# Optimization experiments

Measured on AMD Instinct MI355X. Metric: run time of the kernel, lower is better.

Reference implementation:

```python
import jax, jax.numpy as jnp
import numpy as np
from jax import lax

ACT_SCALE = (0.5, 0.5, 0.5)  # act_scale[0..2], also used as bias_scale
STRIDE = 2
QLEVELS = 127.0  # int8 fake-quant levels (2**7 - 1)


@jax.custom_vjp
def ste_round(x):
    return jnp.round(x)

def _ste_fwd(x):
    return jnp.round(x), None

def _ste_bwd(_, g):
    return (g,)

ste_round.defvjp(_ste_fwd, _ste_bwd)


def fq_act(x, scale):
    # quantize_activations_gemm_A: normalize by scale, clip to [-1,1], 8-bit grid
    return ste_round(jnp.clip(x / scale, -1.0, 1.0) * QLEVELS) / QLEVELS


def qw(w):
    # quantize_weight_gemm_S: per-tensor max-abs scale + 8-bit fake quant
    s = jnp.max(jnp.abs(w))
    wq = ste_round(jnp.clip(w / s, -1.0, 1.0) * QLEVELS) / QLEVELS
    return wq, s


def qb(b):
    # quantize_bias_gemm: round to 1/127 grid
    return ste_round(b * QLEVELS) / QLEVELS


def relu6s(x, scale):
    # ReLU6S: scaled ReLU6
    return jnp.clip(x / scale, 0.0, 6.0)


def conv(x, w, stride=1, pad=0):
    return lax.conv_general_dilated(
        x, w, (stride, stride), [(pad, pad), (pad, pad)],
        dimension_numbers=("NCHW", "OIHW", "NCHW"))


def bottleneck_fwd(x, w1, b1, w2, b2, w3, b3, ws, bs):
    s0, s1, s2a = ACT_SCALE
    x = fq_act(x, s0)
    residual = x
    # conv1: 1x1
    w1q, c1s = qw(w1)
    b1q = qb(b1) / (c1s * s0)
    out = (conv(x, w1q) + b1q[None, :, None, None]) * c1s
    out = relu6s(out, s0) * s0
    out = fq_act(out, s1)
    # conv2: 3x3 stride
    w2q, c2s = qw(w2)
    b2q = qb(b2) / (c2s * s1)
    out = (conv(out, w2q, stride=STRIDE, pad=1) + b2q[None, :, None, None]) * c2s
    out = relu6s(out, s1) * s1
    out = fq_act(out, s2a)
    # conv3: 1x1 (source's padding=1 on a 1x1 conv is a shape bug; dropped)
    w3q, c3s = qw(w3)
    b3q = qb(b3) / (c2s * s2a)  # NOTE: source divides by conv2_scale (preserved)
    out = (conv(out, w3q) + b3q[None, :, None, None]) * c3s
    out = out * s2a
    # downsample shortcut: 1x1 stride
    wsq, css = qw(ws)
    bsq = qb(bs) / (css * s0)
    residual = (conv(residual, wsq, stride=STRIDE) + bsq[None, :, None, None]) * css
    residual = residual * s0
    return jnp.clip(out + residual, 0.0, 6.0)  # final ReLU6


def setup_inputs() -> dict:
    key = jax.random.key(0)
    ks = jax.random.split(key, 9)
    B, Cin, P, H, W = 64, 512, 256, 28, 28
    Cout = 4 * P
    def w_init(k, shape):
        fan_in = shape[1] * shape[2] * shape[3]
        return jax.random.normal(k, shape, jnp.float32) * np.float32(np.sqrt(2.0 / fan_in))
    return {
        "x": jax.random.normal(ks[0], (B, Cin, H, W), jnp.float32),
        "w1": w_init(ks[1], (P, Cin, 1, 1)),
        "b1": jax.random.normal(ks[2], (P,), jnp.float32) * 0.01,
        "w2": w_init(ks[3], (P, P, 3, 3)),
        "b2": jax.random.normal(ks[4], (P,), jnp.float32) * 0.01,
        "w3": w_init(ks[5], (Cout, P, 1, 1)),
        "b3": jax.random.normal(ks[6], (Cout,), jnp.float32) * 0.01,
        "ws": w_init(ks[7], (Cout, Cin, 1, 1)),
        "bs": jax.random.normal(ks[8], (Cout,), jnp.float32) * 0.01,
    }


def reference(x, w1, b1, w2, b2, w3, b3, ws, bs):
    return bottleneck_fwd(x, w1, b1, w2, b2, w3, b3, ws, bs)
```

## Files before the change

### kernel.cpp

```cpp
#include <hip/hip_runtime.h>
#include <stdint.h>

typedef int   int4v __attribute__((ext_vector_type(4)));
typedef float f32x4 __attribute__((ext_vector_type(4)));

#define WS_SCALES 0ull
#define WS_ZERO   256ull
#define WS_BI1    1024ull
#define WS_BI2    2048ull
#define WS_BI3    4096ull
#define WS_BIS    8192ull
#define WS_W1Q    16384ull
#define WS_W2Q    (WS_W1Q + 131072ull)
#define WS_W3Q    (WS_W2Q + 589824ull)
#define WS_WSQ    (WS_W3Q + 262144ull)
#define WS_A0     2097152ull
#define WS_A1     (WS_A0 + 25690112ull)
#define WS_A2     (WS_A1 + 12845056ull)

__device__ __forceinline__ void gll16(const void* g, void* l) {
    __builtin_amdgcn_global_load_lds((const __attribute__((address_space(1))) void*)g,
                                     (__attribute__((address_space(3))) void*)l, 16, 0, 0);
}

#define VMCNT_BAR(n) asm volatile("s_waitcnt vmcnt(" #n ")\n\ts_barrier" ::: "memory")

__global__ void k_init(float* wshead) {
    int i = blockIdx.x * 256 + threadIdx.x;
    wshead[i] = 0.0f;
}

__global__ void k_maxabs(const float* __restrict__ w1, const float* __restrict__ w2,
                         const float* __restrict__ w3, const float* __restrict__ wsd,
                         float* __restrict__ scales) {
    const float* srcs[4] = {w1, w2, w3, wsd};
    const int n4s[4] = {32768, 147456, 65536, 131072};
    int t = blockIdx.y;
    const f32x4* s = (const f32x4*)srcs[t];
    int n4 = n4s[t];
    float m = 0.0f;
    for (int i = blockIdx.x * 256 + threadIdx.x; i < n4; i += gridDim.x * 256) {
        f32x4 v = s[i];
        m = fmaxf(m, fmaxf(fmaxf(fabsf(v[0]), fabsf(v[1])), fmaxf(fabsf(v[2]), fabsf(v[3]))));
    }
    __shared__ float red[256];
    red[threadIdx.x] = m;
    __syncthreads();
    for (int st = 128; st > 0; st >>= 1) {
        if (threadIdx.x < st) red[threadIdx.x] = fmaxf(red[threadIdx.x], red[threadIdx.x + st]);
        __syncthreads();
    }
    if (threadIdx.x == 0) atomicMax((int*)&scales[t], __float_as_int(red[0]));
}

__global__ void k_quant_w(const float* __restrict__ w1, const float* __restrict__ w2,
                          const float* __restrict__ w3, const float* __restrict__ wsd,
                          const float* __restrict__ b1, const float* __restrict__ b2,
                          const float* __restrict__ b3, const float* __restrict__ bs,
                          char* __restrict__ wsb) {
    const float* sc = (const float*)(wsb + WS_SCALES);
    int mode = blockIdx.y;
    int i0 = blockIdx.x * 256 + threadIdx.x;
    int stride = gridDim.x * 256;
    if (mode == 0) {
        float s = sc[0]; signed char* o = (signed char*)(wsb + WS_W1Q);
        for (int i = i0; i < 131072; i += stride)
            o[i] = (signed char)(int)rintf(fminf(fmaxf(w1[i] / s, -1.f), 1.f) * 127.f);
    } else if (mode == 1) {
        float s = sc[1]; signed char* o = (signed char*)(wsb + WS_W2Q);
        for (int i = i0; i < 589824; i += stride) {
            int oo = i / 2304, r2 = i - oo * 2304;
            int c = r2 / 9, kk = r2 - c * 9;
            o[(size_t)oo * 2304 + kk * 256 + c] =
                (signed char)(int)rintf(fminf(fmaxf(w2[i] / s, -1.f), 1.f) * 127.f);
        }
    } else if (mode == 2) {
        float s = sc[2]; signed char* o = (signed char*)(wsb + WS_W3Q);
        for (int i = i0; i < 262144; i += stride)
            o[i] = (signed char)(int)rintf(fminf(fmaxf(w3[i] / s, -1.f), 1.f) * 127.f);
    } else if (mode == 3) {
        float s = sc[3]; signed char* o = (signed char*)(wsb + WS_WSQ);
        for (int i = i0; i < 524288; i += stride)
            o[i] = (signed char)(int)rintf(fminf(fmaxf(wsd[i] / s, -1.f), 1.f) * 127.f);
    } else if (mode == 4) {
        float* o = (float*)(wsb + WS_BI1);
        for (int i = i0; i < 256; i += stride) o[i] = rintf(b1[i] * 127.f);
    } else if (mode == 5) {
        float* o = (float*)(wsb + WS_BI2);
        for (int i = i0; i < 256; i += stride) o[i] = rintf(b2[i] * 127.f);
    } else if (mode == 6) {
        float* o = (float*)(wsb + WS_BI3);
        for (int i = i0; i < 1024; i += stride) o[i] = rintf(b3[i] * 127.f);
    } else {
        float* o = (float*)(wsb + WS_BIS);
        for (int i = i0; i < 1024; i += stride) o[i] = rintf(bs[i] * 127.f);
    }
}

__global__ __launch_bounds__(256) void k_quant_x(const float* __restrict__ x,
                                                 signed char* __restrict__ a0) {
    __shared__ signed char tile[32][132];
    int b = blockIdx.z;
    int p0 = blockIdx.x * 128, c0 = blockIdx.y * 32;
    int tc = threadIdx.x >> 3;
    int pq = (threadIdx.x & 7) * 16;
    const float* xr = x + ((size_t)b * 512 + c0 + tc) * 784 + p0 + pq;
#pragma unroll
    for (int u = 0; u < 4; u++) {
        int p = p0 + pq + u * 4;
        f32x4 v = {0.f, 0.f, 0.f, 0.f};
        if (p < 784) v = *(const f32x4*)(xr + u * 4);
        signed char q[4];
#pragma unroll
        for (int e = 0; e < 4; e++) {
            float f = fminf(fmaxf(v[e] * 2.f, -1.f), 1.f);
            q[e] = (signed char)(int)rintf(f * 127.f);
        }
        *(int*)&tile[tc][pq + u * 4] = *(int*)q;
    }
    __syncthreads();
#pragma unroll
    for (int u = 0; u < 4; u++) {
        int idx = threadIdx.x + u * 256;
        int pp = idx >> 3, cs = (idx & 7) * 4;
        if (p0 + pp < 784) {
            unsigned pk = 0;
#pragma unroll
            for (int i = 0; i < 4; i++)
                pk |= (unsigned)(unsigned char)tile[cs + i][pp] << (8 * i);
            *(unsigned*)(a0 + ((size_t)b * 784 + p0 + pp) * 512 + c0 + cs) = pk;
        }
    }
}

template <int MODE, int BM, int BN, int WGM, int WGN>
__global__ __launch_bounds__(256) void k_conv(char* __restrict__ wsb, float* __restrict__ dout) {
    constexpr int FM = BM / WGM / 16;
    constexpr int FN = BN / WGN / 16;
    constexpr int SB = BN / 16;
    constexpr int NI_B = SB / 4;
    constexpr int KTOT = (MODE == 0) ? 512 : (MODE == 1) ? 2304 : 768;
    constexpr int NSTEP = KTOT / 64;
    constexpr int BMP = BM + 16;
    constexpr int LDS_STAGE = BN * 64;
    constexpr int LDS_EPI = (MODE == 2) ? 64 * (BN + 4) * 4 : BN * BMP;
    constexpr int LDSZ = (3 * LDS_STAGE > LDS_EPI) ? 3 * LDS_STAGE : LDS_EPI;
    static_assert(FM + NI_B == 6 || FM + NI_B == 4, "steady bar count");
    static_assert(FM == 4 || FM == 2, "tail bar count");
    static_assert(NSTEP % 2 == 0, "even steps");

    __shared__ alignas(16) char lds[LDSZ];

    const int tid = threadIdx.x;
    const int wid = tid >> 6;
    const int lane = tid & 63;
    const int n0 = blockIdx.x * BN;
    const int m0 = blockIdx.y * BM;
    const int bb = blockIdx.z;

    const float* sc = (const float*)(wsb + WS_SCALES);
    const int srow = lane >> 2;
    const int lrow = lane & 15;
    const int quad = lane >> 4;
    const int wm = (wid % WGM) * (BM / WGM);
    const int wn = (wid / WGM) * (BN / WGN);
    const int xco = ((lane & 3) ^ ((lane >> 3) & 3)) << 4;
    const char* zp = wsb + WS_ZERO + xco;

    const char* aB[FM];
    const char* aB2[FM];
#pragma unroll
    for (int i = 0; i < FM; i++) {
        int m = m0 + wm + i * 16 + lrow;
        if constexpr (MODE == 0) {
            aB[i] = wsb + WS_W1Q + (size_t)m * 512 + quad * 16;
        } else if constexpr (MODE == 1) {
            aB[i] = wsb + WS_W2Q + (size_t)m * 2304 + quad * 16;
        } else {
            aB[i]  = wsb + WS_W3Q + (size_t)m * 256 + quad * 16;
            aB2[i] = wsb + WS_WSQ + (size_t)m * 512 + quad * 16;
        }
    }

    int4v acc3[FM][FN] = {};
    int4v accS[FM][FN] = {};

    auto srcB = [&](int s, int k0) -> const char* {
        int n = n0 + s * 16 + srow;
        const char* g = zp;
        if constexpr (MODE == 0) {
            g = wsb + WS_A0 + (size_t)n * 512 + k0 + xco;
        } else if constexpr (MODE == 1) {
            unsigned b = (unsigned)n / 196u;
            unsigned hw = (unsigned)n - b * 196u;
            int oh = hw / 14, ow = hw - oh * 14;
            int tap = k0 >> 8;
            int kh = tap / 3, kw = tap - kh * 3;
            int c0 = k0 & 255;
            int ih = 2 * oh - 1 + kh, iw = 2 * ow - 1 + kw;
            if (ih >= 0 && ih < 28 && iw >= 0 && iw < 28)
                g = wsb + WS_A1 + ((size_t)b * 784 + ih * 28 + iw) * 256 + c0 + xco;
        } else {
            if (n < 196) {
                if (k0 < 256) {
                    g = wsb + WS_A2 + ((size_t)bb * 196 + n) * 256 + k0 + xco;
                } else {
                    int oh = n / 14, ow = n - oh * 14;
                    int ps = oh * 56 + ow * 2;
                    g = wsb + WS_A0 + ((size_t)bb * 784 + ps) * 512 + (k0 - 256) + xco;
                }
            }
        }
        return g;
    };

    auto stageB = [&](int t, char* buf) {
        const int k0 = t * 64;
#pragma unroll
        for (int ii = 0; ii < NI_B; ii++) {
            const int s = wid + ii * 4;
            gll16(srcB(s, k0), buf + s * 1024);
        }
    };

    auto loadA = [&](int t, int4v (&a)[FM]) {
        if constexpr (MODE == 2) {
            if (t < 4) {
                const int off = t * 64;
#pragma unroll
                for (int i = 0; i < FM; i++) a[i] = *(const int4v*)(aB[i] + off);
            } else {
                const int off = (t - 4) * 64;
#pragma unroll
                for (int i = 0; i < FM; i++) a[i] = *(const int4v*)(aB2[i] + off);
            }
        } else {
            const int off = t * 64;
#pragma unroll
            for (int i = 0; i < FM; i++) a[i] = *(const int4v*)(aB[i] + off);
        }
    };

    auto dsB = [&](const char* cur, int4v (&b)[FN]) {
#pragma unroll
        for (int j = 0; j < FN; j++) {
            int n = wn + j * 16 + lrow;
            b[j] = *(const int4v*)(cur + n * 64 + ((quad ^ ((n >> 1) & 3)) << 4));
        }
    };

    auto MF = [&](int4v (&ac)[FM][FN], int4v (&a)[FM], int4v (&b)[FN]) {
#pragma unroll
        for (int i = 0; i < FM; i++)
#pragma unroll
            for (int j = 0; j < FN; j++)
                ac[i][j] = __builtin_amdgcn_mfma_i32_16x16x64_i8(a[i], b[j], ac[i][j], 0, 0, 0);
    };

    int4v aC[FM], aN[FM], bfr[FN];
    stageB(0, lds);
    stageB(1, lds + LDS_STAGE);
    loadA(0, aC);
    VMCNT_BAR(0);

    for (int t = 0; t < NSTEP; t += 2) {
        loadA(t + 1, aN);
        __builtin_amdgcn_sched_barrier(0);
        if (t + 2 < NSTEP) stageB(t + 2, lds + ((t + 2) % 3) * LDS_STAGE);
        dsB(lds + (t % 3) * LDS_STAGE, bfr);
        if (MODE != 2 || t < 4) MF(acc3, aC, bfr); else MF(accS, aC, bfr);
        if (t + 1 == NSTEP - 1) {
            if constexpr (FM == 4) VMCNT_BAR(4); else VMCNT_BAR(2);
        } else {
            if constexpr (FM + NI_B == 6) VMCNT_BAR(6); else VMCNT_BAR(4);
        }

        if (t + 2 < NSTEP) loadA(t + 2, aC);
        __builtin_amdgcn_sched_barrier(0);
        if (t + 3 < NSTEP) stageB(t + 3, lds + ((t + 3) % 3) * LDS_STAGE);
        dsB(lds + ((t + 1) % 3) * LDS_STAGE, bfr);
        if (MODE != 2 || t + 1 < 4) MF(acc3, aN, bfr); else MF(accS, aN, bfr);
        if (t + 2 < NSTEP) {
            if constexpr (FM + NI_B == 6) VMCNT_BAR(6); else VMCNT_BAR(4);
        }
    }

    if constexpr (MODE == 0 || MODE == 1) {
        const float alpha = sc[MODE] / 16129.0f;
        const float* bi = (const float*)(wsb + (MODE == 0 ? WS_BI1 : WS_BI2));
        signed char* outp = (signed char*)(wsb + (MODE == 0 ? WS_A1 : WS_A2));
        __syncthreads();
#pragma unroll
        for (int i = 0; i < FM; i++) {
            int mloc = wm + i * 16 + quad * 4;
            int mb = m0 + mloc;
            float bt[4];
#pragma unroll
            for (int r = 0; r < 4; r++) bt[r] = bi[mb + r] * (2.0f / 127.0f);
#pragma unroll
            for (int j = 0; j < FN; j++) {
                int nloc = wn + j * 16 + lrow;
                unsigned pk = 0;
#pragma unroll
                for (int r = 0; r < 4; r++) {
                    float v = alpha * (float)acc3[i][j][r] + bt[r];
                    int q = (int)rintf(127.0f * fminf(fmaxf(2.0f * v, 0.0f), 1.0f));
                    pk |= (unsigned)(q & 0xFF) << (8 * r);
                }
                *(unsigned*)(lds + nloc * BMP + mloc) = pk;
            }
        }
        __syncthreads();
        for (int u = tid; u < BN * (BM / 16); u += 256) {
            int row = u / (BM / 16);
            int seg = u % (BM / 16);
            uint4 v = *(const uint4*)(lds + row * BMP + seg * 16);
            *(uint4*)(outp + (size_t)(n0 + row) * 256 + m0 + seg * 16) = v;
        }
    } else {
        const float c2 = sc[1], c3 = sc[2], cS = sc[3];
        const float* bi3 = (const float*)(wsb + WS_BI3);
        const float* bis = (const float*)(wsb + WS_BIS);
        float* ldsF = (float*)lds;
        constexpr int LDN = BN + 4;
        constexpr int SEGS = BN / 16;
        for (int half = 0; half < 2; half++) {
            __syncthreads();
            if (wm == half * 64) {
#pragma unroll
                for (int i = 0; i < FM; i++) {
                    int mloc = i * 16 + quad * 4;
                    int mg = m0 + half * 64 + mloc;
                    float bt[4];
#pragma unroll
                    for (int r = 0; r < 4; r++)
                        bt[r] = bi3[mg + r] * (c3 / (127.0f * c2)) + bis[mg + r] * (1.0f / 127.0f);
#pragma unroll
                    for (int j = 0; j < FN; j++) {
                        int nloc = wn + j * 16 + lrow;
#pragma unroll
                        for (int r = 0; r < 4; r++) {
                            float v = (c3 * (float)acc3[i][j][r] + cS * (float)accS[i][j][r])
                                          * (0.5f / 16129.0f) + bt[r];
                            v = v < 0.0f ? 0.0f : (v > 6.0f ? 6.0f : v);
                            ldsF[(mloc + r) * LDN + nloc] = v;
                        }
                    }
                }
            }
            __syncthreads();
            {
                int rw0 = tid / SEGS, seg = tid % SEGS;
                int nbase = n0 + seg * 16;
                for (int row = rw0; row < 64; row += 256 / SEGS) {
                    const float* src = ldsF + row * LDN + seg * 16;
                    float* dst = dout + ((size_t)bb * 1024 + m0 + half * 64 + row) * 196 + nbase;
                    if (nbase + 16 <= 196) {
                        *(f32x4*)(dst + 0)  = *(const f32x4*)(src + 0);
                        *(f32x4*)(dst + 4)  = *(const f32x4*)(src + 4);
                        *(f32x4*)(dst + 8)  = *(const f32x4*)(src + 8);
                        *(f32x4*)(dst + 12) = *(const f32x4*)(src + 12);
                    } else {
                        for (int q = 0; q < 16 && nbase + q < 196; q++) dst[q] = src[q];
                    }
                }
            }
        }
    }
}

extern "C" void kernel_launch(void* const* d_in, const int* in_sizes, int n_in,
                              void* d_out, int out_size, void* d_ws, size_t ws_size,
                              hipStream_t stream) {
    const float* x   = (const float*)d_in[0];
    const float* w1  = (const float*)d_in[1];
    const float* b1  = (const float*)d_in[2];
    const float* w2  = (const float*)d_in[3];
    const float* b2  = (const float*)d_in[4];
    const float* w3  = (const float*)d_in[5];
    const float* b3  = (const float*)d_in[6];
    const float* wsd = (const float*)d_in[7];
    const float* bs  = (const float*)d_in[8];
    float* out = (float*)d_out;
    char* wsb = (char*)d_ws;

    k_init<<<16, 256, 0, stream>>>((float*)wsb);
    k_maxabs<<<dim3(128, 4), 256, 0, stream>>>(w1, w2, w3, wsd, (float*)(wsb + WS_SCALES));
    k_quant_w<<<dim3(96, 8), 256, 0, stream>>>(w1, w2, w3, wsd, b1, b2, b3, bs, wsb);
    k_quant_x<<<dim3(7, 16, 64), 256, 0, stream>>>(x, (signed char*)(wsb + WS_A0));
    k_conv<0, 128, 128, 2, 2><<<dim3(392, 2, 1), 256, 0, stream>>>(wsb, out);
    k_conv<1, 64, 128, 2, 2><<<dim3(98, 4, 1), 256, 0, stream>>>(wsb, out);
    k_conv<2, 128, 128, 2, 2><<<dim3(2, 8, 64), 256, 0, stream>>>(wsb, out);
}
```

Measured before the change: 334.9 us.

## Stage whole K in LDS for 1x1 convs; LDS-stage both operands in 3x3 conv

The 1x1 conv kernels (conv1 and conv3+shortcut) now issue every B-tile load for the full K range up front into LDS, wait once, then run all MFMAs with A read straight from global. This drops the hand-tuned triple-buffer pipeline and its per-step waits. The 3x3 conv moves to its own kernel that stages both weights and im2col activations through a triple-buffered LDS ring with a single wait per step. The trade-off is much larger LDS use in the 1x1 kernels (up to 96KB for MODE 2), which lowers occupancy and loses the overlap of loads with compute.

```diff
diff --git a/kernel.cpp b/kernel.cpp
--- a/kernel.cpp
+++ b/kernel.cpp
@@ -134,20 +134,17 @@
 }
 
 template <int MODE, int BM, int BN, int WGM, int WGN>
-__global__ __launch_bounds__(256) void k_conv(char* __restrict__ wsb, float* __restrict__ dout) {
+__global__ __launch_bounds__(256) void k_conv_os(char* __restrict__ wsb, float* __restrict__ dout) {
     constexpr int FM = BM / WGM / 16;
     constexpr int FN = BN / WGN / 16;
-    constexpr int SB = BN / 16;
-    constexpr int NI_B = SB / 4;
-    constexpr int KTOT = (MODE == 0) ? 512 : (MODE == 1) ? 2304 : 768;
+    constexpr int NI_B = BN / 64;
+    constexpr int KTOT = (MODE == 0) ? 512 : 768;
     constexpr int NSTEP = KTOT / 64;
     constexpr int BMP = BM + 16;
     constexpr int LDS_STAGE = BN * 64;
+    constexpr int LDS_ALL = NSTEP * LDS_STAGE;
     constexpr int LDS_EPI = (MODE == 2) ? 64 * (BN + 4) * 4 : BN * BMP;
-    constexpr int LDSZ = (3 * LDS_STAGE > LDS_EPI) ? 3 * LDS_STAGE : LDS_EPI;
-    static_assert(FM + NI_B == 6 || FM + NI_B == 4, "steady bar count");
-    static_assert(FM == 4 || FM == 2, "tail bar count");
-    static_assert(NSTEP % 2 == 0, "even steps");
+    constexpr int LDSZ = (LDS_ALL > LDS_EPI) ? LDS_ALL : LDS_EPI;
 
     __shared__ alignas(16) char lds[LDSZ];
 
@@ -174,56 +171,44 @@
         int m = m0 + wm + i * 16 + lrow;
         if constexpr (MODE == 0) {
             aB[i] = wsb + WS_W1Q + (size_t)m * 512 + quad * 16;
-        } else if constexpr (MODE == 1) {
-            aB[i] = wsb + WS_W2Q + (size_t)m * 2304 + quad * 16;
         } else {
             aB[i]  = wsb + WS_W3Q + (size_t)m * 256 + quad * 16;
             aB2[i] = wsb + WS_WSQ + (size_t)m * 512 + quad * 16;
         }
     }
 
+#pragma unroll
+    for (int t = 0; t < NSTEP; t++) {
+        const int k0 = t * 64;
+#pragma unroll
+        for (int ii = 0; ii < NI_B; ii++) {
+            const int s = wid + ii * 4;
+            int n = n0 + s * 16 + srow;
+            const char* g = zp;
+            if constexpr (MODE == 0) {
+                g = wsb + WS_A0 + (size_t)n * 512 + k0 + xco;
+            } else {
+                if (n < 196) {
+                    if (k0 < 256) {
+                        g = wsb + WS_A2 + ((size_t)bb * 196 + n) * 256 + k0 + xco;
+                    } else {
+                        int oh = n / 14, ow = n - oh * 14;
+                        int ps = oh * 56 + ow * 2;
+                        g = wsb + WS_A0 + ((size_t)bb * 784 + ps) * 512 + (k0 - 256) + xco;
+                    }
+                }
+            }
+            gll16(g, lds + t * LDS_STAGE + s * 1024);
+        }
+    }
+    VMCNT_BAR(0);
+
     int4v acc3[FM][FN] = {};
     int4v accS[FM][FN] = {};
 
-    auto srcB = [&](int s, int k0) -> const char* {
-        int n = n0 + s * 16 + srow;
-        const char* g = zp;
-        if constexpr (MODE == 0) {
-            g = wsb + WS_A0 + (size_t)n * 512 + k0 + xco;
-        } else if constexpr (MODE == 1) {
-            unsigned b = (unsigned)n / 196u;
-            unsigned hw = (unsigned)n - b * 196u;
-            int oh = hw / 14, ow = hw - oh * 14;
-            int tap = k0 >> 8;
-            int kh = tap / 3, kw = tap - kh * 3;
-            int c0 = k0 & 255;
-            int ih = 2 * oh - 1 + kh, iw = 2 * ow - 1 + kw;
-            if (ih >= 0 && ih < 28 && iw >= 0 && iw < 28)
-                g = wsb + WS_A1 + ((size_t)b * 784 + ih * 28 + iw) * 256 + c0 + xco;
-        } else {
-            if (n < 196) {
-                if (k0 < 256) {
-                    g = wsb + WS_A2 + ((size_t)bb * 196 + n) * 256 + k0 + xco;
-                } else {
-                    int oh = n / 14, ow = n - oh * 14;
-                    int ps = oh * 56 + ow * 2;
-                    g = wsb + WS_A0 + ((size_t)bb * 784 + ps) * 512 + (k0 - 256) + xco;
-                }
-            }
-        }
-        return g;
-    };
-
-    auto stageB = [&](int t, char* buf) {
-        const int k0 = t * 64;
-#pragma unroll
-        for (int ii = 0; ii < NI_B; ii++) {
-            const int s = wid + ii * 4;
-            gll16(srcB(s, k0), buf + s * 1024);
-        }
-    };
-
-    auto loadA = [&](int t, int4v (&a)[FM]) {
+#pragma unroll
+    for (int t = 0; t < NSTEP; t++) {
+        int4v a[FM], b[FN];
         if constexpr (MODE == 2) {
             if (t < 4) {
                 const int off = t * 64;
@@ -239,56 +224,31 @@
 #pragma unroll
             for (int i = 0; i < FM; i++) a[i] = *(const int4v*)(aB[i] + off);
         }
-    };
-
-    auto dsB = [&](const char* cur, int4v (&b)[FN]) {
+        const char* cur = lds + t * LDS_STAGE;
 #pragma unroll
         for (int j = 0; j < FN; j++) {
             int n = wn + j * 16 + lrow;
             b[j] = *(const int4v*)(cur + n * 64 + ((quad ^ ((n >> 1) & 3)) << 4));
         }
-    };
-
-    auto MF = [&](int4v (&ac)[FM][FN], int4v (&a)[FM], int4v (&b)[FN]) {
-#pragma unroll
-        for (int i = 0; i < FM; i++)
-#pragma unroll
-            for (int j = 0; j < FN; j++)
-                ac[i][j] = __builtin_amdgcn_mfma_i32_16x16x64_i8(a[i], b[j], ac[i][j], 0, 0, 0);
-    };
-
-    int4v aC[FM], aN[FM], bfr[FN];
-    stageB(0, lds);
-    stageB(1, lds + LDS_STAGE);
-    loadA(0, aC);
-    VMCNT_BAR(0);
-
-    for (int t = 0; t < NSTEP; t += 2) {
-        loadA(t + 1, aN);
-        __builtin_amdgcn_sched_barrier(0);
-        if (t + 2 < NSTEP) stageB(t + 2, lds + ((t + 2) % 3) * LDS_STAGE);
-        dsB(lds + (t % 3) * LDS_STAGE, bfr);
-        if (MODE != 2 || t < 4) MF(acc3, aC, bfr); else MF(accS, aC, bfr);
-        if (t + 1 == NSTEP - 1) {
-            if constexpr (FM == 4) VMCNT_BAR(4); else VMCNT_BAR(2);
+        if (MODE != 2 || t < 4) {
+#pragma unroll
+            for (int i = 0; i < FM; i++)
+#pragma unroll
+                for (int j = 0; j < FN; j++)
+                    acc3[i][j] = __builtin_amdgcn_mfma_i32_16x16x64_i8(a[i], b[j], acc3[i][j], 0, 0, 0);
         } else {
-            if constexpr (FM + NI_B == 6) VMCNT_BAR(6); else VMCNT_BAR(4);
-        }
-
-        if (t + 2 < NSTEP) loadA(t + 2, aC);
-        __builtin_amdgcn_sched_barrier(0);
-        if (t + 3 < NSTEP) stageB(t + 3, lds + ((t + 3) % 3) * LDS_STAGE);
-        dsB(lds + ((t + 1) % 3) * LDS_STAGE, bfr);
-        if (MODE != 2 || t + 1 < 4) MF(acc3, aN, bfr); else MF(accS, aN, bfr);
-        if (t + 2 < NSTEP) {
-            if constexpr (FM + NI_B == 6) VMCNT_BAR(6); else VMCNT_BAR(4);
-        }
-    }
-
-    if constexpr (MODE == 0 || MODE == 1) {
-        const float alpha = sc[MODE] / 16129.0f;
-        const float* bi = (const float*)(wsb + (MODE == 0 ? WS_BI1 : WS_BI2));
-        signed char* outp = (signed char*)(wsb + (MODE == 0 ? WS_A1 : WS_A2));
+#pragma unroll
+            for (int i = 0; i < FM; i++)
+#pragma unroll
+                for (int j = 0; j < FN; j++)
+                    accS[i][j] = __builtin_amdgcn_mfma_i32_16x16x64_i8(a[i], b[j], accS[i][j], 0, 0, 0);
+        }
+    }
+
+    if constexpr (MODE == 0) {
+        const float alpha = sc[0] / 16129.0f;
+        const float* bi = (const float*)(wsb + WS_BI1);
+        signed char* outp = (signed char*)(wsb + WS_A1);
         __syncthreads();
 #pragma unroll
         for (int i = 0; i < FM; i++) {
@@ -369,6 +329,129 @@
     }
 }
 
+__global__ __launch_bounds__(256) void k_conv2(char* __restrict__ wsb) {
+    constexpr int BM = 64, BN = 128, WGM = 2, WGN = 2;
+    constexpr int FM = BM / WGM / 16;
+    constexpr int FN = BN / WGN / 16;
+    constexpr int ISS_A = BM / 16;
+    constexpr int NI = (BM + BN) / 64;
+    constexpr int NSTEP = 2304 / 64;
+    constexpr int BMP = BM + 16;
+    constexpr int LDS_STAGE = (BM + BN) * 64;
+    constexpr int LDS_EPI = BN * BMP;
+    constexpr int LDSZ = 3 * LDS_STAGE;
+
+    __shared__ alignas(16) char lds[LDSZ];
+
+    const int tid = threadIdx.x;
+    const int wid = tid >> 6;
+    const int lane = tid & 63;
+    const int n0 = blockIdx.x * BN;
+    const int m0 = blockIdx.y * BM;
+
+    const float* sc = (const float*)(wsb + WS_SCALES);
+    const int srow = lane >> 2;
+    const int lrow = lane & 15;
+    const int quad = lane >> 4;
+    const int wm = (wid % WGM) * (BM / WGM);
+    const int wn = (wid / WGM) * (BN / WGN);
+    const int xco = ((lane & 3) ^ ((lane >> 3) & 3)) << 4;
+    const char* zp = wsb + WS_ZERO + xco;
+
+    int4v acc[FM][FN] = {};
+
+    auto src_ptr = [&](int s, int k0) -> const char* {
+        const char* g;
+        if (s < ISS_A) {
+            int m = m0 + s * 16 + srow;
+            g = wsb + WS_W2Q + (size_t)m * 2304 + k0 + xco;
+        } else {
+            int n = n0 + (s - ISS_A) * 16 + srow;
+            g = zp;
+            unsigned b = (unsigned)n / 196u;
+            unsigned hw = (unsigned)n - b * 196u;
+            int oh = hw / 14, ow = hw - oh * 14;
+            int tap = k0 >> 8;
+            int kh = tap / 3, kw = tap - kh * 3;
+            int c0 = k0 & 255;
+            int ih = 2 * oh - 1 + kh, iw = 2 * ow - 1 + kw;
+            if (ih >= 0 && ih < 28 && iw >= 0 && iw < 28)
+                g = wsb + WS_A1 + ((size_t)b * 784 + ih * 28 + iw) * 256 + c0 + xco;
+        }
+        return g;
+    };
+
+    auto stage = [&](int t, char* buf) {
+        const int k0 = t * 64;
+#pragma unroll
+        for (int ii = 0; ii < NI; ii++) {
+            const int s = wid + ii * 4;
+            gll16(src_ptr(s, k0), buf + s * 1024);
+        }
+    };
+
+    stage(0, lds);
+    stage(1, lds + LDS_STAGE);
+    for (int t = 0; t < NSTEP; ++t) {
+        char* cur = lds + (t % 3) * LDS_STAGE;
+        if (t == NSTEP - 1) {
+            VMCNT_BAR(0);
+        } else {
+            VMCNT_BAR(3);
+        }
+        if (t + 2 < NSTEP) stage(t + 2, lds + ((t + 2) % 3) * LDS_STAGE);
+
+        int4v afr[FM], bfr[FN];
+#pragma unroll
+        for (int i = 0; i < FM; i++) {
+            int m = wm + i * 16 + lrow;
+            afr[i] = *(const int4v*)(cur + m * 64 + ((quad ^ ((m >> 1) & 3)) << 4));
+        }
+#pragma unroll
+        for (int j = 0; j < FN; j++) {
+            int n = wn + j * 16 + lrow;
+            bfr[j] = *(const int4v*)(cur + (BM + n) * 64 + ((quad ^ ((n >> 1) & 3)) << 4));
+        }
+#pragma unroll
+        for (int i = 0; i < FM; i++)
+#pragma unroll
+            for (int j = 0; j < FN; j++)
+                acc[i][j] = __builtin_amdgcn_mfma_i32_16x16x64_i8(afr[i], bfr[j], acc[i][j], 0, 0, 0);
+    }
+
+    const float alpha = sc[1] / 16129.0f;
+    const float* bi = (const float*)(wsb + WS_BI2);
+    signed char* outp = (signed char*)(wsb + WS_A2);
+    __syncthreads();
+#pragma unroll
+    for (int i = 0; i < FM; i++) {
+        int mloc = wm + i * 16 + quad * 4;
+        int mb = m0 + mloc;
+        float bt[4];
+#pragma unroll
+        for (int r = 0; r < 4; r++) bt[r] = bi[mb + r] * (2.0f / 127.0f);
+#pragma unroll
+        for (int j = 0; j < FN; j++) {
+            int nloc = wn + j * 16 + lrow;
+            unsigned pk = 0;
+#pragma unroll
+            for (int r = 0; r < 4; r++) {
+                float v = alpha * (float)acc[i][j][r] + bt[r];
+                int q = (int)rintf(127.0f * fminf(fmaxf(2.0f * v, 0.0f), 1.0f));
+                pk |= (unsigned)(q & 0xFF) << (8 * r);
+            }
+            *(unsigned*)(lds + nloc * BMP + mloc) = pk;
+        }
+    }
+    __syncthreads();
+    for (int u = tid; u < BN * (BM / 16); u += 256) {
+        int row = u / (BM / 16);
+        int seg = u % (BM / 16);
+        uint4 v = *(const uint4*)(lds + row * BMP + seg * 16);
+        *(uint4*)(outp + (size_t)(n0 + row) * 256 + m0 + seg * 16) = v;
+    }
+}
+
 extern "C" void kernel_launch(void* const* d_in, const int* in_sizes, int n_in,
                               void* d_out, int out_size, void* d_ws, size_t ws_size,
                               hipStream_t stream) {
@@ -388,7 +471,7 @@
     k_maxabs<<<dim3(128, 4), 256, 0, stream>>>(w1, w2, w3, wsd, (float*)(wsb + WS_SCALES));
     k_quant_w<<<dim3(96, 8), 256, 0, stream>>>(w1, w2, w3, wsd, b1, b2, b3, bs, wsb);
     k_quant_x<<<dim3(7, 16, 64), 256, 0, stream>>>(x, (signed char*)(wsb + WS_A0));
-    k_conv<0, 128, 128, 2, 2><<<dim3(392, 2, 1), 256, 0, stream>>>(wsb, out);
-    k_conv<1, 64, 128, 2, 2><<<dim3(98, 4, 1), 256, 0, stream>>>(wsb, out);
-    k_conv<2, 128, 128, 2, 2><<<dim3(2, 8, 64), 256, 0, stream>>>(wsb, out);
-}
+    k_conv_os<0, 128, 128, 2, 2><<<dim3(392, 2, 1), 256, 0, stream>>>(wsb, out);
+    k_conv2<<<dim3(98, 4, 1), 256, 0, stream>>>(wsb);
+    k_conv_os<2, 128, 128, 2, 2><<<dim3(2, 8, 64), 256, 0, stream>>>(wsb, out);
+}
```

Measured after the change: 333.9 us. No clear change (-0.3%).
